# Performance work log

Measured on AMD Instinct MI355X. Metric: run time of the kernel, lower is better.

## Reference

```python
import jax, jax.numpy as jnp
import numpy as np

T, D, E = 65536, 1024, 64  # tokens, d_model, n_experts

def setup_inputs() -> dict:
    key = jax.random.key(0)
    k1, k2 = jax.random.split(key)
    x = jax.random.normal(k1, (T, D), dtype=jnp.float32)
    Wg = jax.random.normal(k2, (D, E), dtype=jnp.float32) * (1.0 / np.sqrt(D))
    return {"x": x, "Wg": Wg, "top_k": 2}

def reference(x, Wg, top_k):
    # Token-to-expert gating: logits -> softmax -> top-k -> renormalized combine weights.
    logits = jnp.einsum('td,de->te', x, Wg)            # [T, E]
    probs = jax.nn.softmax(logits, axis=-1)            # [T, E]
    topk_vals, topk_idx = jax.lax.top_k(probs, top_k)  # [T, k], [T, k]
    combine = topk_vals / jnp.sum(topk_vals, axis=-1, keepdims=True)  # renormalize over selected experts
    return combine, topk_idx, probs
```

## Files before the change

### kernel.cpp

```cpp
#include <hip/hip_runtime.h>
#include <hip/hip_bf16.h>
#include <math.h>


#define D_DIM 1024
#define E_DIM 64
#define TM    64
#define KC    64
#define NCH   (D_DIM / KC)
#define TPB   256
#define MARGIN 1e-3f
#define WT_U4  16384

typedef float f32x4 __attribute__((ext_vector_type(4)));
typedef short s16x8 __attribute__((ext_vector_type(8)));

__device__ __forceinline__ ushort bf16u(float f) {
  union { __hip_bfloat16 b; ushort u; } cv;
  cv.b = __float2bfloat16(f);
  return cv.u;
}

__global__ void wprep_kernel(const float* __restrict__ Wg, uint4* __restrict__ w4,
                             unsigned* __restrict__ ctr) {
  const int gi = blockIdx.x * blockDim.x + threadIdx.x;
  if (gi == 0) ctr[0] = 0u;
  const int ch = gi >> 9;
  const int e  = (gi >> 3) & 63;
  const int g  = gi & 7;
  const int k0 = ch * KC + g * 8;
  unsigned hp[4], lp[4];
#pragma unroll
  for (int jj = 0; jj < 4; ++jj) {
    const float w0 = Wg[(k0 + 2 * jj    ) * E_DIM + e];
    const float w1 = Wg[(k0 + 2 * jj + 1) * E_DIM + e];
    const unsigned h0 = (unsigned)bf16u(w0) << 16;
    const unsigned h1 = (unsigned)bf16u(w1) << 16;
    const float l0 = w0 - __uint_as_float(h0);
    const float l1 = w1 - __uint_as_float(h1);
    hp[jj] = (h1) | (h0 >> 16);
    lp[jj] = ((unsigned)bf16u(l1) << 16) | (unsigned)bf16u(l0);
  }
  w4[gi]        = make_uint4(hp[0], hp[1], hp[2], hp[3]);
  w4[8192 + gi] = make_uint4(lp[0], lp[1], lp[2], lp[3]);
}

struct Frag2 { s16x8 hi, lo; };

__device__ __forceinline__ Frag2 cvt8(const float4 a, const float4 b) {
  const float f[8] = {a.x, a.y, a.z, a.w, b.x, b.y, b.z, b.w};
  Frag2 r;
#pragma unroll
  for (int i = 0; i < 8; ++i) {
    const ushort h = bf16u(f[i]);
    r.hi[i] = (short)h;
    const float lf = f[i] - __uint_as_float((unsigned)h << 16);
    r.lo[i] = (short)bf16u(lf);
  }
  return r;
}

__global__ __launch_bounds__(TPB, 4) void router_mfma(
    const float* __restrict__ x, const uint4* __restrict__ wt,
    float* __restrict__ out, unsigned* __restrict__ ctr,
    unsigned* __restrict__ list, int rcap, int T)
{
  const int tid   = threadIdx.x;
  const int wid   = tid >> 6;
  const int lane  = tid & 63;
  const int c     = lane & 15;
  const int q     = lane >> 4;
  const int tok   = blockIdx.x * TM + wid * 16 + c;

  f32x4 acc[4];
#pragma unroll
  for (int et = 0; et < 4; ++et) acc[et] = (f32x4){0.f, 0.f, 0.f, 0.f};

  const float* __restrict__ xb = x + (size_t)tok * D_DIM + q * 8;
  const uint4* __restrict__ wl = wt + c * 8 + q;

  float4 xA[4], xB[4];
#pragma unroll
  for (int v = 0; v < 4; ++v) {
    const int s = v >> 1, h = v & 1;
    xA[v] = *(const float4*)(xb + s * 32 + h * 4);
    xB[v] = *(const float4*)(xb + KC + s * 32 + h * 4);
  }

  auto step = [&](float4 (&xr)[4], int ch) {
    s16x8 a0h[4], a0l[4];
#pragma unroll
    for (int et = 0; et < 4; ++et) {
      a0h[et] = *(const s16x8*)(wl + (size_t)ch * 512 + et * 128);
      a0l[et] = *(const s16x8*)(wl + (size_t)ch * 512 + 8192 + et * 128);
    }
    const Frag2 b0 = cvt8(xr[0], xr[1]);
    const Frag2 b1 = cvt8(xr[2], xr[3]);
#pragma unroll
    for (int et = 0; et < 4; ++et) {
      f32x4 a = acc[et];
      a = __builtin_amdgcn_mfma_f32_16x16x32_bf16(a0h[et], b0.hi, a, 0, 0, 0);
      a = __builtin_amdgcn_mfma_f32_16x16x32_bf16(a0h[et], b0.lo, a, 0, 0, 0);
      a = __builtin_amdgcn_mfma_f32_16x16x32_bf16(a0l[et], b0.hi, a, 0, 0, 0);
      acc[et] = a;
    }
    if (ch + 2 < NCH) {
#pragma unroll
      for (int v = 0; v < 4; ++v) {
        const int s = v >> 1, h = v & 1;
        xr[v] = *(const float4*)(xb + (ch + 2) * KC + s * 32 + h * 4);
      }
    }
    s16x8 a1h[4], a1l[4];
#pragma unroll
    for (int et = 0; et < 4; ++et) {
      a1h[et] = *(const s16x8*)(wl + (size_t)ch * 512 + et * 128 + 4);
      a1l[et] = *(const s16x8*)(wl + (size_t)ch * 512 + 8192 + et * 128 + 4);
    }
#pragma unroll
    for (int et = 0; et < 4; ++et) {
      f32x4 a = acc[et];
      a = __builtin_amdgcn_mfma_f32_16x16x32_bf16(a1h[et], b1.hi, a, 0, 0, 0);
      a = __builtin_amdgcn_mfma_f32_16x16x32_bf16(a1h[et], b1.lo, a, 0, 0, 0);
      a = __builtin_amdgcn_mfma_f32_16x16x32_bf16(a1l[et], b1.hi, a, 0, 0, 0);
      acc[et] = a;
    }
  };

  for (int ch = 0; ch < NCH; ch += 2) {
    step(xA, ch);
    step(xB, ch + 1);
  }

  const size_t Ts = (size_t)T;
  float* const comb = out;
  float* const idxo = out + 2 * Ts;
  float* const prob = out + 4 * Ts;

  float v[16];
#pragma unroll
  for (int et = 0; et < 4; ++et)
#pragma unroll
    for (int r = 0; r < 4; ++r) v[et * 4 + r] = acc[et][r];

  float v1 = v[0], v2 = -INFINITY, v3 = -INFINITY;
  int   i1 = q * 4, i2 = 0;
#pragma unroll
  for (int et = 0; et < 4; ++et)
#pragma unroll
    for (int r = 0; r < 4; ++r) {
      if (et == 0 && r == 0) continue;
      const float p  = v[et * 4 + r];
      const int   ei = et * 16 + q * 4 + r;
      if (p > v1)      { v3 = v2; v2 = v1; i2 = i1; v1 = p; i1 = ei; }
      else if (p > v2) { v3 = v2; v2 = p;  i2 = ei; }
      else if (p > v3) { v3 = p; }
    }
#pragma unroll
  for (int d = 16; d <= 32; d <<= 1) {
    const float ov1 = __shfl_xor(v1, d); const int oi1 = __shfl_xor(i1, d);
    const float ov2 = __shfl_xor(v2, d); const int oi2 = __shfl_xor(i2, d);
    const float ov3 = __shfl_xor(v3, d);
    const bool  ob1 = (ov1 > v1) || (ov1 == v1 && oi1 < i1);
    const float w1v = ob1 ? ov1 : v1;  const int w1i = ob1 ? oi1 : i1;
    const float l1v = ob1 ? v1  : ov1; const int l1i = ob1 ? i1  : oi1;
    const float w2v = ob1 ? ov2 : v2;  const int w2i = ob1 ? oi2 : i2;
    const float ls2 = ob1 ? v2  : ov2;
    const float ws3 = ob1 ? ov3 : v3;
    const bool  b2  = (l1v > w2v) || (l1v == w2v && l1i < w2i);
    const float a2v = b2 ? l1v : w2v; const int a2i = b2 ? l1i : w2i;
    const float a3v = b2 ? fmaxf(w2v, ls2) : fmaxf(l1v, ws3);
    v1 = w1v; i1 = w1i; v2 = a2v; i2 = a2i; v3 = a3v;
  }

  float s = 0.f;
#pragma unroll
  for (int i = 0; i < 16; ++i) { v[i] = __expf(v[i] - v1); s += v[i]; }
  s += __shfl_xor(s, 16);
  s += __shfl_xor(s, 32);
  const float inv = 1.f / s;

#pragma unroll
  for (int et = 0; et < 4; ++et)
    *(float4*)&prob[(size_t)tok * E_DIM + et * 16 + q * 4] =
        make_float4(v[et * 4 + 0] * inv, v[et * 4 + 1] * inv,
                    v[et * 4 + 2] * inv, v[et * 4 + 3] * inv);

  if (q == 0) {
    if ((v1 - v2 < MARGIN) || (v2 - v3 < MARGIN)) {
      const unsigned slot = atomicAdd(ctr, 1u);
      if ((int)slot < rcap) list[slot] = (unsigned)tok;
    }
    const float c1 = 1.f / (1.f + __expf(v2 - v1));
    *(float2*)&comb[2 * (size_t)tok] = make_float2(c1, 1.f - c1);
    *(float2*)&idxo[2 * (size_t)tok] = make_float2((float)i1, (float)i2);
  }
}

__global__ __launch_bounds__(256) void repair_kernel(
    const float* __restrict__ x, const float* __restrict__ Wg,
    float* __restrict__ out, const unsigned* __restrict__ ctr,
    const unsigned* __restrict__ list, int rcap, int T)
{
  __shared__ double part[4][E_DIM];
  const int tid = threadIdx.x;
  const int e   = tid & 63;
  const int s   = tid >> 6;
  const unsigned total = ctr[0];
  const unsigned n = total < (unsigned)rcap ? total : (unsigned)rcap;

  for (unsigned j = blockIdx.x; j < n; j += gridDim.x) {
    const int t = (int)list[j];
    const float* xr = x  + (size_t)t * D_DIM + s * 256;
    const float* wr = Wg + (size_t)(s * 256) * E_DIM + e;
    double a = 0.0;
#pragma unroll 8
    for (int d = 0; d < 256; ++d)
      a += (double)xr[d] * (double)wr[(size_t)d * E_DIM];
    part[s][e] = a;
    __syncthreads();
    if (tid < 64) {
      const float l = (float)(part[0][e] + part[1][e] + part[2][e] + part[3][e]);
      float m = l;
#pragma unroll
      for (int d2 = 1; d2 < 64; d2 <<= 1) m = fmaxf(m, __shfl_xor(m, d2));
      const float p = expf(l - m);
      float ss = p;
#pragma unroll
      for (int d2 = 1; d2 < 64; d2 <<= 1) ss += __shfl_xor(ss, d2);
      out[4 * (size_t)T + (size_t)t * E_DIM + e] = p / ss;
      float v1 = l, v2 = -INFINITY; int i1 = e, i2 = 0;
#pragma unroll
      for (int d2 = 1; d2 < 64; d2 <<= 1) {
        const float ov1 = __shfl_xor(v1, d2); const int oi1 = __shfl_xor(i1, d2);
        const float ov2 = __shfl_xor(v2, d2); const int oi2 = __shfl_xor(i2, d2);
        const bool  ob1 = (ov1 > v1) || (ov1 == v1 && oi1 < i1);
        const float w1v = ob1 ? ov1 : v1;  const int w1i = ob1 ? oi1 : i1;
        const float l1v = ob1 ? v1  : ov1; const int l1i = ob1 ? i1  : oi1;
        const float w2v = ob1 ? ov2 : v2;  const int w2i = ob1 ? oi2 : i2;
        const bool  b2  = (l1v > w2v) || (l1v == w2v && l1i < w2i);
        v1 = w1v; i1 = w1i;
        v2 = b2 ? l1v : w2v; i2 = b2 ? l1i : w2i;
      }
      if (e == 0) {
        const float c1 = 1.f / (1.f + expf(v2 - v1));
        out[2 * (size_t)t]     = c1;
        out[2 * (size_t)t + 1] = 1.f - c1;
        out[2 * (size_t)T + 2 * (size_t)t]     = (float)i1;
        out[2 * (size_t)T + 2 * (size_t)t + 1] = (float)i2;
      }
    }
    __syncthreads();
  }
}

extern "C" void kernel_launch(void* const* d_in, const int* in_sizes, int n_in,
                              void* d_out, int out_size, void* d_ws, size_t ws_size,
                              hipStream_t stream) {
  const float* x  = (const float*)d_in[0];
  const float* Wg = (const float*)d_in[1];
  float* out = (float*)d_out;
  uint4* wt  = (uint4*)d_ws;
  unsigned* ctr  = (unsigned*)d_ws + WT_U4 * 4;
  unsigned* list = ctr + 1;
  const int T = in_sizes[0] / D_DIM;

  long avail = ((long)ws_size - (long)(WT_U4 * 16 + 4)) / 4;
  int rcap = avail < 0 ? 0 : (avail > 8192 ? 8192 : (int)avail);

  wprep_kernel<<<dim3(NCH * E_DIM * 8 / TPB), dim3(TPB), 0, stream>>>(Wg, wt, ctr);
  router_mfma<<<dim3(T / TM), dim3(TPB), 0, stream>>>(x, wt, out, ctr, list, rcap, T);
  repair_kernel<<<dim3(1024), dim3(256), 0, stream>>>(x, Wg, out, ctr, list, rcap, T);
}
```

Baseline: 474.8 us.

## Stage gate weights through double-buffered LDS with XOR-swizzled layout

Each chunk of the prepared bf16 hi/lo weights is now loaded cooperatively by the whole block into a double-buffered shared-memory tile, prefetched through registers one chunk ahead. Previously every wave read weights directly from global memory. The weight prep kernel permutes 8-element groups with an XOR swizzle so the per-lane LDS fragment reads avoid bank conflicts. The cost is 32KB of LDS per block, which may limit occupancy, and a block-wide barrier on every chunk.

Result: faster. 429.1 us (-9.6%).

```diff
diff --git a/kernel.cpp b/kernel.cpp
--- a/kernel.cpp
+++ b/kernel.cpp
@@ -28,7 +28,7 @@
   const int ch = gi >> 9;
   const int e  = (gi >> 3) & 63;
   const int g  = gi & 7;
-  const int k0 = ch * KC + g * 8;
+  const int k0 = ch * KC + (g ^ (e & 7)) * 8;
   unsigned hp[4], lp[4];
 #pragma unroll
   for (int jj = 0; jj < 4; ++jj) {
@@ -38,7 +38,7 @@
     const unsigned h1 = (unsigned)bf16u(w1) << 16;
     const float l0 = w0 - __uint_as_float(h0);
     const float l1 = w1 - __uint_as_float(h1);
-    hp[jj] = (h1) | (h0 >> 16);
+    hp[jj] = h1 | (h0 >> 16);
     lp[jj] = ((unsigned)bf16u(l1) << 16) | (unsigned)bf16u(l0);
   }
   w4[gi]        = make_uint4(hp[0], hp[1], hp[2], hp[3]);
@@ -65,6 +65,8 @@
     float* __restrict__ out, unsigned* __restrict__ ctr,
     unsigned* __restrict__ list, int rcap, int T)
 {
+  __shared__ uint4 sw[2][1024];
+
   const int tid   = threadIdx.x;
   const int wid   = tid >> 6;
   const int lane  = tid & 63;
@@ -77,33 +79,44 @@
   for (int et = 0; et < 4; ++et) acc[et] = (f32x4){0.f, 0.f, 0.f, 0.f};
 
   const float* __restrict__ xb = x + (size_t)tok * D_DIM + q * 8;
-  const uint4* __restrict__ wl = wt + c * 8 + q;
-
+
+  uint4  wr[4];
   float4 xA[4], xB[4];
+
+#pragma unroll
+  for (int i = 0; i < 4; ++i) wr[i] = wt[(i >> 1) * 8192 + (i & 1) * 256 + tid];
+#pragma unroll
+  for (int i = 0; i < 4; ++i) sw[0][(i >> 1) * 512 + (i & 1) * 256 + tid] = wr[i];
+#pragma unroll
+  for (int i = 0; i < 4; ++i) wr[i] = wt[(i >> 1) * 8192 + 512 + (i & 1) * 256 + tid];
 #pragma unroll
   for (int v = 0; v < 4; ++v) {
     const int s = v >> 1, h = v & 1;
     xA[v] = *(const float4*)(xb + s * 32 + h * 4);
     xB[v] = *(const float4*)(xb + KC + s * 32 + h * 4);
   }
-
-  auto step = [&](float4 (&xr)[4], int ch) {
-    s16x8 a0h[4], a0l[4];
-#pragma unroll
-    for (int et = 0; et < 4; ++et) {
-      a0h[et] = *(const s16x8*)(wl + (size_t)ch * 512 + et * 128);
-      a0l[et] = *(const s16x8*)(wl + (size_t)ch * 512 + 8192 + et * 128);
-    }
+  __syncthreads();
+
+  const int row0 = c * 64;
+  const int g0 = ((0 + q) ^ (c & 7)) * 8;
+  const int g1 = ((4 + q) ^ (c & 7)) * 8;
+
+  auto stepf = [&](float4 (&xr)[4], int ch) {
+    const int cur = ch & 1;
+    if (ch + 1 < NCH) {
+#pragma unroll
+      for (int i = 0; i < 4; ++i)
+        sw[cur ^ 1][(i >> 1) * 512 + (i & 1) * 256 + tid] = wr[i];
+    }
+    if (ch + 2 < NCH) {
+#pragma unroll
+      for (int i = 0; i < 4; ++i)
+        wr[i] = wt[(i >> 1) * 8192 + (ch + 2) * 512 + (i & 1) * 256 + tid];
+    }
+
     const Frag2 b0 = cvt8(xr[0], xr[1]);
     const Frag2 b1 = cvt8(xr[2], xr[3]);
-#pragma unroll
-    for (int et = 0; et < 4; ++et) {
-      f32x4 a = acc[et];
-      a = __builtin_amdgcn_mfma_f32_16x16x32_bf16(a0h[et], b0.hi, a, 0, 0, 0);
-      a = __builtin_amdgcn_mfma_f32_16x16x32_bf16(a0h[et], b0.lo, a, 0, 0, 0);
-      a = __builtin_amdgcn_mfma_f32_16x16x32_bf16(a0l[et], b0.hi, a, 0, 0, 0);
-      acc[et] = a;
-    }
+
     if (ch + 2 < NCH) {
 #pragma unroll
       for (int v = 0; v < 4; ++v) {
@@ -111,25 +124,38 @@
         xr[v] = *(const float4*)(xb + (ch + 2) * KC + s * 32 + h * 4);
       }
     }
-    s16x8 a1h[4], a1l[4];
-#pragma unroll
-    for (int et = 0; et < 4; ++et) {
-      a1h[et] = *(const s16x8*)(wl + (size_t)ch * 512 + et * 128 + 4);
-      a1l[et] = *(const s16x8*)(wl + (size_t)ch * 512 + 8192 + et * 128 + 4);
-    }
-#pragma unroll
-    for (int et = 0; et < 4; ++et) {
-      f32x4 a = acc[et];
-      a = __builtin_amdgcn_mfma_f32_16x16x32_bf16(a1h[et], b1.hi, a, 0, 0, 0);
-      a = __builtin_amdgcn_mfma_f32_16x16x32_bf16(a1h[et], b1.lo, a, 0, 0, 0);
-      a = __builtin_amdgcn_mfma_f32_16x16x32_bf16(a1l[et], b1.hi, a, 0, 0, 0);
-      acc[et] = a;
-    }
+
+    const ushort* bufh = (const ushort*)&sw[cur][0];
+    const ushort* bufl = bufh + 4096;
+#pragma unroll
+    for (int s = 0; s < 2; ++s) {
+      const int go = s ? g1 : g0;
+      const Frag2& bs = s ? b1 : b0;
+      s16x8 ah[4];
+#pragma unroll
+      for (int et = 0; et < 4; ++et)
+        ah[et] = *(const s16x8*)(bufh + et * 1024 + row0 + go);
+#pragma unroll
+      for (int et = 0; et < 4; ++et) {
+        f32x4 a = acc[et];
+        a = __builtin_amdgcn_mfma_f32_16x16x32_bf16(ah[et], bs.hi, a, 0, 0, 0);
+        a = __builtin_amdgcn_mfma_f32_16x16x32_bf16(ah[et], bs.lo, a, 0, 0, 0);
+        acc[et] = a;
+      }
+      s16x8 al[4];
+#pragma unroll
+      for (int et = 0; et < 4; ++et)
+        al[et] = *(const s16x8*)(bufl + et * 1024 + row0 + go);
+#pragma unroll
+      for (int et = 0; et < 4; ++et)
+        acc[et] = __builtin_amdgcn_mfma_f32_16x16x32_bf16(al[et], bs.hi, acc[et], 0, 0, 0);
+    }
+    __syncthreads();
   };
 
   for (int ch = 0; ch < NCH; ch += 2) {
-    step(xA, ch);
-    step(xB, ch + 1);
+    stepf(xA, ch);
+    stepf(xB, ch + 1);
   }
 
   const size_t Ts = (size_t)T;
```

## Stage x and weight tiles through LDS with async global-to-LDS double buffering

Applied to the files above, without the earlier changes.

Replaces the per-lane direct global loads of x rows and weight fragments with async global_load_lds copies into double-buffered, XOR-swizzled shared memory tiles of 32-wide K chunks. The weight prep is reorganized so hi/lo planes are laid out per chunk with a matching swizzle for conflict-free LDS reads. The change aims to make global reads coalesced and to overlap the next chunk's loads with the current MFMAs, at the cost of a block-wide barrier every chunk and twice as many loop iterations.

Result: faster. 411.1 us (-13.4%).

```diff
diff --git a/kernel.cpp b/kernel.cpp
--- a/kernel.cpp
+++ b/kernel.cpp
@@ -6,8 +6,8 @@
 #define D_DIM 1024
 #define E_DIM 64
 #define TM    64
-#define KC    64
-#define NCH   (D_DIM / KC)
+#define BK    32
+#define NCH   (D_DIM / BK)
 #define TPB   256
 #define MARGIN 1e-3f
 #define WT_U4  16384
@@ -21,28 +21,36 @@
   return cv.u;
 }
 
+__device__ __forceinline__ void async_cp16(void* l, const void* g) {
+  __builtin_amdgcn_global_load_lds(
+      (const __attribute__((address_space(1))) void*)g,
+      (__attribute__((address_space(3))) void*)l, 16, 0, 0);
+}
+
 __global__ void wprep_kernel(const float* __restrict__ Wg, uint4* __restrict__ w4,
                              unsigned* __restrict__ ctr) {
   const int gi = blockIdx.x * blockDim.x + threadIdx.x;
   if (gi == 0) ctr[0] = 0u;
-  const int ch = gi >> 9;
-  const int e  = (gi >> 3) & 63;
-  const int g  = gi & 7;
-  const int k0 = ch * KC + g * 8;
-  unsigned hp[4], lp[4];
+  const int p    = gi >> 13;
+  const int ch   = (gi >> 8) & 31;
+  const int e    = (gi >> 2) & 63;
+  const int slot = gi & 3;
+  const int g    = slot ^ ((e >> 1) & 3);
+  const int k0   = ch * BK + g * 8;
+  unsigned pk[4];
 #pragma unroll
   for (int jj = 0; jj < 4; ++jj) {
     const float w0 = Wg[(k0 + 2 * jj    ) * E_DIM + e];
     const float w1 = Wg[(k0 + 2 * jj + 1) * E_DIM + e];
-    const unsigned h0 = (unsigned)bf16u(w0) << 16;
-    const unsigned h1 = (unsigned)bf16u(w1) << 16;
-    const float l0 = w0 - __uint_as_float(h0);
-    const float l1 = w1 - __uint_as_float(h1);
-    hp[jj] = (h1) | (h0 >> 16);
-    lp[jj] = ((unsigned)bf16u(l1) << 16) | (unsigned)bf16u(l0);
-  }
-  w4[gi]        = make_uint4(hp[0], hp[1], hp[2], hp[3]);
-  w4[8192 + gi] = make_uint4(lp[0], lp[1], lp[2], lp[3]);
+    if (p == 0) {
+      pk[jj] = ((unsigned)bf16u(w1) << 16) | (unsigned)bf16u(w0);
+    } else {
+      const float l0 = w0 - __uint_as_float((unsigned)bf16u(w0) << 16);
+      const float l1 = w1 - __uint_as_float((unsigned)bf16u(w1) << 16);
+      pk[jj] = ((unsigned)bf16u(l1) << 16) | (unsigned)bf16u(l0);
+    }
+  }
+  w4[gi] = make_uint4(pk[0], pk[1], pk[2], pk[3]);
 }
 
 struct Frag2 { s16x8 hi, lo; };
@@ -65,71 +73,77 @@
     float* __restrict__ out, unsigned* __restrict__ ctr,
     unsigned* __restrict__ list, int rcap, int T)
 {
-  const int tid   = threadIdx.x;
-  const int wid   = tid >> 6;
-  const int lane  = tid & 63;
-  const int c     = lane & 15;
-  const int q     = lane >> 4;
-  const int tok   = blockIdx.x * TM + wid * 16 + c;
+  __shared__ uint4 sx[2][512];
+  __shared__ uint4 sw[2][512];
+
+  const int tid  = threadIdx.x;
+  const int wid  = tid >> 6;
+  const int lane = tid & 63;
+  const int c    = lane & 15;
+  const int q    = lane >> 4;
+  const int trow = wid * 16 + c;
+  const int tok  = blockIdx.x * TM + trow;
+  const size_t xbase = (size_t)blockIdx.x * TM * D_DIM;
 
   f32x4 acc[4];
 #pragma unroll
   for (int et = 0; et < 4; ++et) acc[et] = (f32x4){0.f, 0.f, 0.f, 0.f};
 
-  const float* __restrict__ xb = x + (size_t)tok * D_DIM + q * 8;
-  const uint4* __restrict__ wl = wt + c * 8 + q;
-
-  float4 xA[4], xB[4];
-#pragma unroll
-  for (int v = 0; v < 4; ++v) {
-    const int s = v >> 1, h = v & 1;
-    xA[v] = *(const float4*)(xb + s * 32 + h * 4);
-    xB[v] = *(const float4*)(xb + KC + s * 32 + h * 4);
-  }
-
-  auto step = [&](float4 (&xr)[4], int ch) {
-    s16x8 a0h[4], a0l[4];
+  const int j0 = wid * 2;
+
+  auto stage = [&](int ch, int buf) {
+#pragma unroll
+    for (int i = 0; i < 2; ++i) {
+      const int j    = j0 + i;
+      const int rowr = j * 8 + (lane >> 3);
+      const float* src = x + xbase + (size_t)rowr * D_DIM + ch * BK
+                       + (((lane & 7) ^ (lane >> 3)) << 2);
+      async_cp16(&sx[buf][j * 64], src);
+    }
+#pragma unroll
+    for (int i = 0; i < 2; ++i) {
+      const int j = j0 + i;
+      const int G = j * 64 + lane;
+      const int p = G >> 8, r = G & 255;
+      const uint4* src = wt + (size_t)(p * 32 + ch) * 256 + r;
+      async_cp16(&sw[buf][j * 64], src);
+    }
+  };
+
+  stage(0, 0);
+  __syncthreads();
+
+  for (int ch = 0; ch < NCH; ++ch) {
+    const int cur = ch & 1;
+    if (ch + 1 < NCH) stage(ch + 1, cur ^ 1);
+
+    const float4* xb4 = (const float4*)&sx[cur][0];
+    const int rb = trow * 8, key = c & 7;
+    const float4 x0 = xb4[rb + ((2 * q + 0) ^ key)];
+    const float4 x1 = xb4[rb + ((2 * q + 1) ^ key)];
+    const Frag2 b = cvt8(x0, x1);
+
+    const s16x8* wb = (const s16x8*)&sw[cur][0];
+    const int slotr = q ^ ((c >> 1) & 3);
+    s16x8 ah[4], al[4];
 #pragma unroll
     for (int et = 0; et < 4; ++et) {
-      a0h[et] = *(const s16x8*)(wl + (size_t)ch * 512 + et * 128);
-      a0l[et] = *(const s16x8*)(wl + (size_t)ch * 512 + 8192 + et * 128);
-    }
-    const Frag2 b0 = cvt8(xr[0], xr[1]);
-    const Frag2 b1 = cvt8(xr[2], xr[3]);
+      const int e = et * 16 + c;
+      ah[et] = wb[e * 4 + slotr];
+      al[et] = wb[256 + e * 4 + slotr];
+    }
 #pragma unroll
     for (int et = 0; et < 4; ++et) {
       f32x4 a = acc[et];
-      a = __builtin_amdgcn_mfma_f32_16x16x32_bf16(a0h[et], b0.hi, a, 0, 0, 0);
-      a = __builtin_amdgcn_mfma_f32_16x16x32_bf16(a0h[et], b0.lo, a, 0, 0, 0);
-      a = __builtin_amdgcn_mfma_f32_16x16x32_bf16(a0l[et], b0.hi, a, 0, 0, 0);
+      a = __builtin_amdgcn_mfma_f32_16x16x32_bf16(ah[et], b.hi, a, 0, 0, 0);
+      a = __builtin_amdgcn_mfma_f32_16x16x32_bf16(ah[et], b.lo, a, 0, 0, 0);
       acc[et] = a;
     }
-    if (ch + 2 < NCH) {
-#pragma unroll
-      for (int v = 0; v < 4; ++v) {
-        const int s = v >> 1, h = v & 1;
-        xr[v] = *(const float4*)(xb + (ch + 2) * KC + s * 32 + h * 4);
-      }
-    }
-    s16x8 a1h[4], a1l[4];
-#pragma unroll
-    for (int et = 0; et < 4; ++et) {
-      a1h[et] = *(const s16x8*)(wl + (size_t)ch * 512 + et * 128 + 4);
-      a1l[et] = *(const s16x8*)(wl + (size_t)ch * 512 + 8192 + et * 128 + 4);
-    }
-#pragma unroll
-    for (int et = 0; et < 4; ++et) {
-      f32x4 a = acc[et];
-      a = __builtin_amdgcn_mfma_f32_16x16x32_bf16(a1h[et], b1.hi, a, 0, 0, 0);
-      a = __builtin_amdgcn_mfma_f32_16x16x32_bf16(a1h[et], b1.lo, a, 0, 0, 0);
-      a = __builtin_amdgcn_mfma_f32_16x16x32_bf16(a1l[et], b1.hi, a, 0, 0, 0);
-      acc[et] = a;
-    }
-  };
-
-  for (int ch = 0; ch < NCH; ch += 2) {
-    step(xA, ch);
-    step(xB, ch + 1);
+#pragma unroll
+    for (int et = 0; et < 4; ++et)
+      acc[et] = __builtin_amdgcn_mfma_f32_16x16x32_bf16(al[et], b.hi, acc[et], 0, 0, 0);
+
+    __syncthreads();
   }
 
   const size_t Ts = (size_t)T;
@@ -268,7 +282,7 @@
   long avail = ((long)ws_size - (long)(WT_U4 * 16 + 4)) / 4;
   int rcap = avail < 0 ? 0 : (avail > 8192 ? 8192 : (int)avail);
 
-  wprep_kernel<<<dim3(NCH * E_DIM * 8 / TPB), dim3(TPB), 0, stream>>>(Wg, wt, ctr);
+  wprep_kernel<<<dim3(WT_U4 / TPB), dim3(TPB), 0, stream>>>(Wg, wt, ctr);
   router_mfma<<<dim3(T / TM), dim3(TPB), 0, stream>>>(x, wt, out, ctr, list, rcap, T);
   repair_kernel<<<dim3(1024), dim3(256), 0, stream>>>(x, Wg, out, ctr, list, rcap, T);
 }
```
